# Kernel optimization log

Measured on AMD Instinct MI355X. Metric: run time of the kernel, lower is better.

## Reference

```python
import jax, jax.numpy as jnp
import numpy as np

B = 65536
IN = 512
HID = 512
NQ = 8
NGATES = 4  # input, forget, output, cell


def setup_inputs() -> dict:
    key = jax.random.key(0)
    ks = jax.random.split(key, 7)
    fan1 = IN + HID
    return {
        "x": jax.random.normal(ks[0], (B, IN), dtype=jnp.float32),
        "h": jax.random.normal(ks[1], (B, HID), dtype=jnp.float32),
        "c": jax.random.normal(ks[2], (B, HID), dtype=jnp.float32),
        # stacked params for the 4 gate networks (PyTorch Linear layout: [out, in])
        "W1": jax.random.normal(ks[3], (NGATES, NQ, fan1), dtype=jnp.float32) / np.sqrt(fan1).astype(np.float32),
        "b1": jax.random.normal(ks[4], (NGATES, NQ), dtype=jnp.float32) * 0.01,
        "W2": jax.random.normal(ks[5], (NGATES, HID, NQ), dtype=jnp.float32) / np.sqrt(NQ).astype(np.float32),
        "b2": jax.random.normal(ks[6], (NGATES, HID), dtype=jnp.float32) * 0.01,
    }


def reference(x, h, c, W1, b1, W2, b2):
    # combined: [B, IN+HID]
    combined = jnp.concatenate([x, h], axis=-1)
    # batched first layer over the 4 gates: [B, 4, NQ]
    z = jnp.tanh(jnp.einsum("bi,gqi->bgq", combined, W1) + b1)
    # batched second layer: [B, 4, HID], sigmoid on ALL gates (incl. cell gate, per source)
    gates = jax.nn.sigmoid(jnp.einsum("bgq,ghq->bgh", z, W2) + b2)
    i, f, o, g = gates[:, 0], gates[:, 1], gates[:, 2], gates[:, 3]
    c_new = f * c + i * g
    h_new = o * jnp.tanh(c_new)
    return h_new, c_new
```

## Files before the change

kernel.cpp:

```cpp
#include <hip/hip_runtime.h>
#include <math.h>

#define B_TOTAL 65536
#define IN_DIM 512
#define HID_DIM 512
#define FAN1 1024
#define NQ 8
#define NGATES 4

__global__ __launch_bounds__(256, 4)
void k1_gemv(const float* __restrict__ x, const float* __restrict__ h,
             const float* __restrict__ W1, const float* __restrict__ b1,
             float* __restrict__ Z) {
    __shared__ __align__(16) float tile[64][64];

    const int tid     = threadIdx.x;
    const int lane    = tid & 63;
    const int g       = __builtin_amdgcn_readfirstlane(tid >> 6);
    const int rowbase = blockIdx.x * 64;

    float acc[8];
#pragma unroll
    for (int j = 0; j < 8; ++j) acc[j] = 0.0f;

    for (int kc = 0; kc < FAN1; kc += 64) {
        const float* src = (kc < IN_DIM) ? (x + kc) : (h + (kc - IN_DIM));

        __syncthreads();
#pragma unroll
        for (int i = 0; i < 4; ++i) {
            int idx = tid + 256 * i;
            int r   = idx >> 4;
            int kg  = idx & 15;
            float4 v = *(const float4*)(src + (size_t)(rowbase + r) * 512 + kg * 4);
            *(float4*)&tile[r][(kg ^ (r & 7)) << 2] = v;
        }
        __syncthreads();

#pragma unroll 2
        for (int kg = 0; kg < 16; ++kg) {
            float4 cv = *(const float4*)&tile[lane][(kg ^ (lane & 7)) << 2];
#pragma unroll
            for (int j = 0; j < 8; ++j) {
                float4 wv = *(const float4*)(W1 + (size_t)(g * 8 + j) * FAN1 + kc + kg * 4);
                acc[j] = fmaf(cv.x, wv.x, acc[j]);
                acc[j] = fmaf(cv.y, wv.y, acc[j]);
                acc[j] = fmaf(cv.z, wv.z, acc[j]);
                acc[j] = fmaf(cv.w, wv.w, acc[j]);
            }
        }
    }

    float o[8];
#pragma unroll
    for (int j = 0; j < 8; ++j) {
        o[j] = tanhf(acc[j] + b1[g * 8 + j]);
    }
    float* zp = Z + (size_t)(rowbase + lane) * 32 + g * 8;
    *(float4*)(zp + 0) = make_float4(o[0], o[1], o[2], o[3]);
    *(float4*)(zp + 4) = make_float4(o[4], o[5], o[6], o[7]);
}

__device__ __forceinline__ float sigmoid_f(float v) {
    return 1.0f / (1.0f + __expf(-v));
}
__device__ __forceinline__ float tanh_fast(float v) {
    return 1.0f - 2.0f / (__expf(2.0f * v) + 1.0f);
}

__global__ __launch_bounds__(256, 4)
void k2_gates(const float* __restrict__ Z, const float* __restrict__ c,
              const float* __restrict__ W2, const float* __restrict__ b2,
              float* __restrict__ out) {
    const int tid     = threadIdx.x;
    const int rowbase = blockIdx.x * 64;

    float w2r[2][4][8];
    float b2r[2][4];
#pragma unroll
    for (int hi = 0; hi < 2; ++hi) {
        int hh = tid + 256 * hi;
#pragma unroll
        for (int g = 0; g < 4; ++g) {
            const float* wp = W2 + (size_t)(g * HID_DIM + hh) * NQ;
            float4 a = *(const float4*)(wp + 0);
            float4 b = *(const float4*)(wp + 4);
            w2r[hi][g][0] = a.x; w2r[hi][g][1] = a.y;
            w2r[hi][g][2] = a.z; w2r[hi][g][3] = a.w;
            w2r[hi][g][4] = b.x; w2r[hi][g][5] = b.y;
            w2r[hi][g][6] = b.z; w2r[hi][g][7] = b.w;
            b2r[hi][g] = b2[g * HID_DIM + hh];
        }
    }

    const size_t c_off = (size_t)B_TOTAL * HID_DIM;

    for (int r = 0; r < 64; ++r) {
        const int row = rowbase + r;
        const float* zrow = Z + (size_t)row * 32;
        float zz[32];
#pragma unroll
        for (int t = 0; t < 8; ++t) {
            float4 zv = *(const float4*)(zrow + 4 * t);
            zz[4 * t + 0] = zv.x; zz[4 * t + 1] = zv.y;
            zz[4 * t + 2] = zv.z; zz[4 * t + 3] = zv.w;
        }
#pragma unroll
        for (int hi = 0; hi < 2; ++hi) {
            int hh = tid + 256 * hi;
            float cv = c[(size_t)row * HID_DIM + hh];
            float pre[4];
#pragma unroll
            for (int g = 0; g < 4; ++g) {
                float a = b2r[hi][g];
#pragma unroll
                for (int q = 0; q < 8; ++q)
                    a = fmaf(zz[g * 8 + q], w2r[hi][g][q], a);
                pre[g] = a;
            }
            float ig = sigmoid_f(pre[0]);
            float fg = sigmoid_f(pre[1]);
            float og = sigmoid_f(pre[2]);
            float gg = sigmoid_f(pre[3]);
            float cn = fg * cv + ig * gg;
            float hn = og * tanh_fast(cn);
            out[(size_t)row * HID_DIM + hh]         = hn;
            out[c_off + (size_t)row * HID_DIM + hh] = cn;
        }
    }
}

extern "C" void kernel_launch(void* const* d_in, const int* in_sizes, int n_in,
                              void* d_out, int out_size, void* d_ws, size_t ws_size,
                              hipStream_t stream) {
    const float* x  = (const float*)d_in[0];
    const float* h  = (const float*)d_in[1];
    const float* c  = (const float*)d_in[2];
    const float* W1 = (const float*)d_in[3];
    const float* b1 = (const float*)d_in[4];
    const float* W2 = (const float*)d_in[5];
    const float* b2 = (const float*)d_in[6];
    float* out = (float*)d_out;
    float* Z   = (float*)d_ws;

    hipLaunchKernelGGL(k1_gemv, dim3(B_TOTAL / 64), dim3(256), 0, stream,
                       x, h, W1, b1, Z);
    hipLaunchKernelGGL(k2_gates, dim3(B_TOTAL / 64), dim3(256), 0, stream,
                       Z, c, W2, b2, out);
}
```

Baseline: 647.2 us.

## Fuse gate GEMV and LSTM cell update into one kernel with LDS-staged weights

Merges the two kernels so the tanh'd first-layer activations stay in shared memory instead of round-tripping through a global workspace. W1 chunks are staged into LDS, and the next x/h and W1 chunks are register-prefetched while the current one is computed. The second stage now handles two hidden columns per thread with vectorized c loads and output stores, plus a one-iteration c prefetch. The costs are more registers and LDS per block, which may reduce occupancy under the 4-blocks launch bound.

```diff
diff --git a/kernel.cpp b/kernel.cpp
--- a/kernel.cpp
+++ b/kernel.cpp
@@ -8,41 +8,87 @@
 #define NQ 8
 #define NGATES 4
 
+__device__ __forceinline__ float sigmoid_f(float v) {
+    return 1.0f / (1.0f + __expf(-v));
+}
+__device__ __forceinline__ float tanh_fast(float v) {
+    return 1.0f - 2.0f / (__expf(2.0f * v) + 1.0f);
+}
+
 __global__ __launch_bounds__(256, 4)
-void k1_gemv(const float* __restrict__ x, const float* __restrict__ h,
-             const float* __restrict__ W1, const float* __restrict__ b1,
-             float* __restrict__ Z) {
+void lstm_fused(const float* __restrict__ x, const float* __restrict__ h,
+                const float* __restrict__ c,
+                const float* __restrict__ W1, const float* __restrict__ b1,
+                const float* __restrict__ W2, const float* __restrict__ b2,
+                float* __restrict__ out) {
     __shared__ __align__(16) float tile[64][64];
-
-    const int tid     = threadIdx.x;
-    const int lane    = tid & 63;
-    const int g       = __builtin_amdgcn_readfirstlane(tid >> 6);
+    __shared__ __align__(16) float w1s[32][64];
+    __shared__ __align__(16) float zs[64][36];
+
+    const int tid  = threadIdx.x;
+    const int lane = tid & 63;
+    const int g    = __builtin_amdgcn_readfirstlane(tid >> 6);
     const int rowbase = blockIdx.x * 64;
 
+    const int srow = tid >> 4;
+    const int skg  = tid & 15;
+
     float acc[8];
 #pragma unroll
     for (int j = 0; j < 8; ++j) acc[j] = 0.0f;
 
+    float4 tReg[4];
+    float4 wReg[2];
+
+    {
+        const float* src = x;
+#pragma unroll
+        for (int i = 0; i < 4; ++i) {
+            int r = srow + 16 * i;
+            tReg[i] = *(const float4*)(src + (size_t)(rowbase + r) * 512 + skg * 4);
+        }
+#pragma unroll
+        for (int i = 0; i < 2; ++i) {
+            int o = srow + 16 * i;
+            wReg[i] = *(const float4*)(W1 + (size_t)o * FAN1 + skg * 4);
+        }
+    }
+
     for (int kc = 0; kc < FAN1; kc += 64) {
-        const float* src = (kc < IN_DIM) ? (x + kc) : (h + (kc - IN_DIM));
-
         __syncthreads();
 #pragma unroll
         for (int i = 0; i < 4; ++i) {
-            int idx = tid + 256 * i;
-            int r   = idx >> 4;
-            int kg  = idx & 15;
-            float4 v = *(const float4*)(src + (size_t)(rowbase + r) * 512 + kg * 4);
-            *(float4*)&tile[r][(kg ^ (r & 7)) << 2] = v;
+            int r = srow + 16 * i;
+            *(float4*)&tile[r][(skg ^ (r & 7)) << 2] = tReg[i];
+        }
+#pragma unroll
+        for (int i = 0; i < 2; ++i) {
+            int o = srow + 16 * i;
+            *(float4*)&w1s[o][skg << 2] = wReg[i];
         }
         __syncthreads();
 
-#pragma unroll 2
+        const int kn = kc + 64;
+        if (kn < FAN1) {
+            const float* src = (kn < IN_DIM) ? (x + kn) : (h + (kn - IN_DIM));
+#pragma unroll
+            for (int i = 0; i < 4; ++i) {
+                int r = srow + 16 * i;
+                tReg[i] = *(const float4*)(src + (size_t)(rowbase + r) * 512 + skg * 4);
+            }
+#pragma unroll
+            for (int i = 0; i < 2; ++i) {
+                int o = srow + 16 * i;
+                wReg[i] = *(const float4*)(W1 + (size_t)o * FAN1 + kn + skg * 4);
+            }
+        }
+
+#pragma unroll
         for (int kg = 0; kg < 16; ++kg) {
             float4 cv = *(const float4*)&tile[lane][(kg ^ (lane & 7)) << 2];
 #pragma unroll
             for (int j = 0; j < 8; ++j) {
-                float4 wv = *(const float4*)(W1 + (size_t)(g * 8 + j) * FAN1 + kc + kg * 4);
+                float4 wv = *(const float4*)&w1s[g * 8 + j][kg << 2];
                 acc[j] = fmaf(cv.x, wv.x, acc[j]);
                 acc[j] = fmaf(cv.y, wv.y, acc[j]);
                 acc[j] = fmaf(cv.z, wv.z, acc[j]);
@@ -51,82 +97,100 @@
         }
     }
 
-    float o[8];
-#pragma unroll
-    for (int j = 0; j < 8; ++j) {
-        o[j] = tanhf(acc[j] + b1[g * 8 + j]);
-    }
-    float* zp = Z + (size_t)(rowbase + lane) * 32 + g * 8;
-    *(float4*)(zp + 0) = make_float4(o[0], o[1], o[2], o[3]);
-    *(float4*)(zp + 4) = make_float4(o[4], o[5], o[6], o[7]);
-}
-
-__device__ __forceinline__ float sigmoid_f(float v) {
-    return 1.0f / (1.0f + __expf(-v));
-}
-__device__ __forceinline__ float tanh_fast(float v) {
-    return 1.0f - 2.0f / (__expf(2.0f * v) + 1.0f);
-}
-
-__global__ __launch_bounds__(256, 4)
-void k2_gates(const float* __restrict__ Z, const float* __restrict__ c,
-              const float* __restrict__ W2, const float* __restrict__ b2,
-              float* __restrict__ out) {
-    const int tid     = threadIdx.x;
-    const int rowbase = blockIdx.x * 64;
-
-    float w2r[2][4][8];
-    float b2r[2][4];
-#pragma unroll
-    for (int hi = 0; hi < 2; ++hi) {
-        int hh = tid + 256 * hi;
-#pragma unroll
-        for (int g = 0; g < 4; ++g) {
-            const float* wp = W2 + (size_t)(g * HID_DIM + hh) * NQ;
-            float4 a = *(const float4*)(wp + 0);
-            float4 b = *(const float4*)(wp + 4);
-            w2r[hi][g][0] = a.x; w2r[hi][g][1] = a.y;
-            w2r[hi][g][2] = a.z; w2r[hi][g][3] = a.w;
-            w2r[hi][g][4] = b.x; w2r[hi][g][5] = b.y;
-            w2r[hi][g][6] = b.z; w2r[hi][g][7] = b.w;
-            b2r[hi][g] = b2[g * HID_DIM + hh];
-        }
-    }
+    {
+        const float* bp = b1 + g * 8;
+        float t0 = tanhf(acc[0] + bp[0]);
+        float t1 = tanhf(acc[1] + bp[1]);
+        float t2 = tanhf(acc[2] + bp[2]);
+        float t3 = tanhf(acc[3] + bp[3]);
+        float t4 = tanhf(acc[4] + bp[4]);
+        float t5 = tanhf(acc[5] + bp[5]);
+        float t6 = tanhf(acc[6] + bp[6]);
+        float t7 = tanhf(acc[7] + bp[7]);
+        *(float4*)&zs[lane][g * 8 + 0] = make_float4(t0, t1, t2, t3);
+        *(float4*)&zs[lane][g * 8 + 4] = make_float4(t4, t5, t6, t7);
+    }
+
+    const int hh = tid * 2;
+    float w2r[4][16];
+    float b2r[4][2];
+#pragma unroll
+    for (int g2 = 0; g2 < 4; ++g2) {
+        const float* wp = W2 + ((size_t)g2 * HID_DIM + hh) * NQ;
+        float4 p0 = *(const float4*)(wp + 0);
+        float4 p1 = *(const float4*)(wp + 4);
+        float4 p2 = *(const float4*)(wp + 8);
+        float4 p3 = *(const float4*)(wp + 12);
+        w2r[g2][0]  = p0.x; w2r[g2][1]  = p0.y; w2r[g2][2]  = p0.z; w2r[g2][3]  = p0.w;
+        w2r[g2][4]  = p1.x; w2r[g2][5]  = p1.y; w2r[g2][6]  = p1.z; w2r[g2][7]  = p1.w;
+        w2r[g2][8]  = p2.x; w2r[g2][9]  = p2.y; w2r[g2][10] = p2.z; w2r[g2][11] = p2.w;
+        w2r[g2][12] = p3.x; w2r[g2][13] = p3.y; w2r[g2][14] = p3.z; w2r[g2][15] = p3.w;
+        float2 bb = *(const float2*)(b2 + (size_t)g2 * HID_DIM + hh);
+        b2r[g2][0] = bb.x; b2r[g2][1] = bb.y;
+    }
+
+    __syncthreads();
 
     const size_t c_off = (size_t)B_TOTAL * HID_DIM;
-
-    for (int r = 0; r < 64; ++r) {
-        const int row = rowbase + r;
-        const float* zrow = Z + (size_t)row * 32;
-        float zz[32];
-#pragma unroll
-        for (int t = 0; t < 8; ++t) {
-            float4 zv = *(const float4*)(zrow + 4 * t);
-            zz[4 * t + 0] = zv.x; zz[4 * t + 1] = zv.y;
-            zz[4 * t + 2] = zv.z; zz[4 * t + 3] = zv.w;
-        }
-#pragma unroll
-        for (int hi = 0; hi < 2; ++hi) {
-            int hh = tid + 256 * hi;
-            float cv = c[(size_t)row * HID_DIM + hh];
-            float pre[4];
-#pragma unroll
-            for (int g = 0; g < 4; ++g) {
-                float a = b2r[hi][g];
-#pragma unroll
-                for (int q = 0; q < 8; ++q)
-                    a = fmaf(zz[g * 8 + q], w2r[hi][g][q], a);
-                pre[g] = a;
-            }
-            float ig = sigmoid_f(pre[0]);
-            float fg = sigmoid_f(pre[1]);
-            float og = sigmoid_f(pre[2]);
-            float gg = sigmoid_f(pre[3]);
-            float cn = fg * cv + ig * gg;
-            float hn = og * tanh_fast(cn);
-            out[(size_t)row * HID_DIM + hh]         = hn;
-            out[c_off + (size_t)row * HID_DIM + hh] = cn;
-        }
+    const float* crow = c   + (size_t)rowbase * HID_DIM + hh;
+    float*       orow = out + (size_t)rowbase * HID_DIM + hh;
+
+    float2 cA = *(const float2*)(crow);
+    float2 cB = *(const float2*)(crow + HID_DIM);
+
+#pragma unroll 1
+    for (int r = 0; r < 64; r += 2) {
+        float2 cN0 = cA, cN1 = cB;
+        if (r + 2 < 64) {
+            cN0 = *(const float2*)(crow + (size_t)(r + 2) * HID_DIM);
+            cN1 = *(const float2*)(crow + (size_t)(r + 3) * HID_DIM);
+        }
+#pragma unroll
+        for (int rr = 0; rr < 2; ++rr) {
+            const int row = r + rr;
+            const float2 cv = rr ? cB : cA;
+            const float* zr = &zs[row][0];
+            float pre0[4], pre1[4];
+#pragma unroll
+            for (int g2 = 0; g2 < 4; ++g2) {
+                float4 za = *(const float4*)(zr + g2 * 8);
+                float4 zb = *(const float4*)(zr + g2 * 8 + 4);
+                float a0 = b2r[g2][0], a1 = b2r[g2][1];
+                a0 = fmaf(za.x, w2r[g2][0], a0);
+                a0 = fmaf(za.y, w2r[g2][1], a0);
+                a0 = fmaf(za.z, w2r[g2][2], a0);
+                a0 = fmaf(za.w, w2r[g2][3], a0);
+                a0 = fmaf(zb.x, w2r[g2][4], a0);
+                a0 = fmaf(zb.y, w2r[g2][5], a0);
+                a0 = fmaf(zb.z, w2r[g2][6], a0);
+                a0 = fmaf(zb.w, w2r[g2][7], a0);
+                a1 = fmaf(za.x, w2r[g2][8], a1);
+                a1 = fmaf(za.y, w2r[g2][9], a1);
+                a1 = fmaf(za.z, w2r[g2][10], a1);
+                a1 = fmaf(za.w, w2r[g2][11], a1);
+                a1 = fmaf(zb.x, w2r[g2][12], a1);
+                a1 = fmaf(zb.y, w2r[g2][13], a1);
+                a1 = fmaf(zb.z, w2r[g2][14], a1);
+                a1 = fmaf(zb.w, w2r[g2][15], a1);
+                pre0[g2] = a0; pre1[g2] = a1;
+            }
+            float ig0 = sigmoid_f(pre0[0]);
+            float fg0 = sigmoid_f(pre0[1]);
+            float og0 = sigmoid_f(pre0[2]);
+            float gg0 = sigmoid_f(pre0[3]);
+            float ig1 = sigmoid_f(pre1[0]);
+            float fg1 = sigmoid_f(pre1[1]);
+            float og1 = sigmoid_f(pre1[2]);
+            float gg1 = sigmoid_f(pre1[3]);
+            float cn0 = fg0 * cv.x + ig0 * gg0;
+            float cn1 = fg1 * cv.y + ig1 * gg1;
+            float hn0 = og0 * tanh_fast(cn0);
+            float hn1 = og1 * tanh_fast(cn1);
+            size_t ob = (size_t)row * HID_DIM;
+            *(float2*)(orow + ob)         = make_float2(hn0, hn1);
+            *(float2*)(orow + c_off + ob) = make_float2(cn0, cn1);
+        }
+        cA = cN0; cB = cN1;
     }
 }
 
@@ -141,10 +205,7 @@
     const float* W2 = (const float*)d_in[5];
     const float* b2 = (const float*)d_in[6];
     float* out = (float*)d_out;
-    float* Z   = (float*)d_ws;
-
-    hipLaunchKernelGGL(k1_gemv, dim3(B_TOTAL / 64), dim3(256), 0, stream,
-                       x, h, W1, b1, Z);
-    hipLaunchKernelGGL(k2_gates, dim3(B_TOTAL / 64), dim3(256), 0, stream,
-                       Z, c, W2, b2, out);
-}
+
+    hipLaunchKernelGGL(lstm_fused, dim3(B_TOTAL / 64), dim3(256), 0, stream,
+                       x, h, c, W1, b1, W2, b2, out);
+}
```

Result: slower. 726.7 us (+12.3%).
